# Kernel optimization log

Measured on AMD Instinct MI355X. Metric: run time of the kernel, lower is better.

The kernel has to match this reference:

```python
import jax, jax.numpy as jnp
import numpy as np

B, T, W_IN = 64, 512, 40
KS = 3
N = KS * KS          # 9 sampling points
CF = 8               # conv filters
GH = 32              # GRU hidden
GIN = (W_IN - KS + 1) * CF  # 304
ATTN = 32


def setup_inputs() -> dict:
    key = jax.random.key(0)
    ks = jax.random.split(key, 10)
    p = {}
    p["x"] = jax.random.normal(ks[0], (B, 1, T, W_IN), jnp.float32)
    p["p_w"] = jax.random.normal(ks[1], (2 * N, 1, KS, KS), jnp.float32) * 0.01
    p["p_b"] = jnp.zeros((2 * N,), jnp.float32)
    p["dcn_w"] = jax.random.normal(ks[2], (CF, 1, KS, KS), jnp.float32) * 0.1
    p["dcn_b"] = jnp.zeros((CF,), jnp.float32)
    p["w_ih"] = jax.random.normal(ks[3], (3 * GH, GIN), jnp.float32) * 0.05
    p["w_hh"] = jax.random.normal(ks[4], (3 * GH, GH), jnp.float32) * 0.05
    p["b_ih"] = jnp.zeros((3 * GH,), jnp.float32)
    p["b_hh"] = jnp.zeros((3 * GH,), jnp.float32)
    p["w1"] = jax.random.normal(ks[5], (ATTN, GH), jnp.float32) * 0.1
    p["b1"] = jnp.zeros((ATTN,), jnp.float32)
    p["w2"] = jax.random.normal(ks[6], (GH, ATTN), jnp.float32) * 0.1
    p["b2"] = jnp.zeros((GH,), jnp.float32)
    p["w3"] = jax.random.normal(ks[7], (2, GH), jnp.float32) * 0.1
    p["b3"] = jnp.zeros((2,), jnp.float32)
    return p


def _deform_conv(x, p_w, p_b, w, b):
    # x: (B,1,H,W). Deform-conv v1: offsets from a VALID 3x3 conv, bilinear gather.
    Bb, C, H, W = x.shape
    offset = jax.lax.conv_general_dilated(
        x, p_w, (1, 1), "VALID",
        dimension_numbers=("NCHW", "OIHW", "NCHW")) + p_b[None, :, None, None]
    h, w_ = offset.shape[2], offset.shape[3]  # (T-2, 38)
    r = KS // 2
    pny, pnx = jnp.meshgrid(jnp.arange(-r, r + 1), jnp.arange(-r, r + 1), indexing="ij")
    p0y, p0x = jnp.meshgrid(jnp.arange(1, h + 1), jnp.arange(1, w_ + 1), indexing="ij")
    py = offset[:, :N] + pny.reshape(1, N, 1, 1) + p0y[None, None]  # (B,N,h,w)
    px = offset[:, N:] + pnx.reshape(1, N, 1, 1) + p0x[None, None]
    py = jnp.clip(py, 0.0, H - 1.0)
    px = jnp.clip(px, 0.0, W - 1.0)
    y0 = jnp.floor(py).astype(jnp.int32)
    x0 = jnp.floor(px).astype(jnp.int32)
    y1 = jnp.minimum(y0 + 1, H - 1)
    x1 = jnp.minimum(x0 + 1, W - 1)
    wy = (py - y0)[:, None]  # (B,1,N,h,w)
    wx = (px - x0)[:, None]
    flat = x.reshape(Bb, C, H * W)

    def gather(yi, xi):
        idx = (yi * W + xi).reshape(Bb, 1, -1)
        g = jnp.take_along_axis(flat, idx, axis=2)
        return g.reshape(Bb, C, N, h, w_)

    g00 = gather(y0, x0); g01 = gather(y0, x1)
    g10 = gather(y1, x0); g11 = gather(y1, x1)
    samp = (g00 * (1 - wy) * (1 - wx) + g01 * (1 - wy) * wx
            + g10 * wy * (1 - wx) + g11 * wy * wx)  # (B,C,N,h,w)
    out = jnp.einsum("bcnhw,ocn->bohw", samp, w.reshape(w.shape[0], C, N))
    return out + b[None, :, None, None]


def _gru(seq, w_ih, w_hh, b_ih, b_hh):
    # seq: (T,B,GIN); PyTorch GRU equations, single layer, h0 = 0
    xp = jnp.einsum("tbi,hi->tbh", seq, w_ih) + b_ih  # (T,B,3H)
    h0 = jnp.zeros((seq.shape[1], GH), seq.dtype)

    def step(hprev, xt):
        hp = hprev @ w_hh.T + b_hh
        xr, xz, xn = jnp.split(xt, 3, axis=-1)
        hr, hz, hn = jnp.split(hp, 3, axis=-1)
        rg = jax.nn.sigmoid(xr + hr)
        zg = jax.nn.sigmoid(xz + hz)
        ng = jnp.tanh(xn + rg * hn)
        hnew = (1 - zg) * ng + zg * hprev
        return hnew, hnew

    _, ys = jax.lax.scan(step, h0, xp)
    return ys  # (T,B,GH)


def _forward(x, p_w, p_b, dcn_w, dcn_b, w_ih, w_hh, b_ih, b_hh, w1, b1, w2, b2, w3, b3):
    y = _deform_conv(x, p_w, p_b, dcn_w, dcn_b)        # (B,CF,h,w)
    h = y.shape[2]
    y = jnp.transpose(y, (2, 0, 3, 1)).reshape(h, y.shape[1], -1)  # wait
    return y


def _model(x, p_w, p_b, dcn_w, dcn_b, w_ih, w_hh, b_ih, b_hh, w1, b1, w2, b2, w3, b3):
    y = _deform_conv(x, p_w, p_b, dcn_w, dcn_b)        # (B,CF,h,w)
    Bb = y.shape[0]
    h = y.shape[2]
    seq = jnp.transpose(y, (2, 0, 3, 1)).reshape(h, Bb, -1)  # (h,B,w*CF) w-major then channel
    enc = jnp.transpose(_gru(seq, w_ih, w_hh, b_ih, b_hh), (1, 0, 2))  # (B,h,GH)
    a = jnp.tanh(enc @ w1.T + b1) @ w2.T + b2          # (B,h,GH)
    a = jax.nn.softmax(a, axis=1)                      # softmax over time
    pooled = jnp.sum(a * enc, axis=1)                  # (B,GH)
    return pooled @ w3.T + b3                          # (B,2)


def reference(x, p_w, p_b, dcn_w, dcn_b, w_ih, w_hh, b_ih, b_hh, w1, b1, w2, b2, w3, b3):
    return _model(x, p_w, p_b, dcn_w, dcn_b, w_ih, w_hh, b_ih, b_hh, w1, b1, w2, b2, w3, b3)
```

## Files before the change

kernel.cpp:

```cpp
#include <hip/hip_runtime.h>
#include <math.h>
#include <stdint.h>

#define BB 64
#define TT 512
#define W_IN 40
#define CF 8
#define GH 32
#define HOUT 510
#define WOUT 38
#define GIN 304
#define G3 96
#define ATT 32
#define MROWS (HOUT * BB)

#define LOG2E 1.4426950408889634f

__device__ __forceinline__ float fast_rcp(float x) {
#if defined(__has_builtin)
# if __has_builtin(__builtin_amdgcn_rcpf)
    return __builtin_amdgcn_rcpf(x);
# else
    return 1.f / x;
# endif
#else
    return 1.f / x;
#endif
}

__device__ __forceinline__ float fast_exp2(float x) {
#if defined(__has_builtin)
# if __has_builtin(__builtin_amdgcn_exp2f)
    return __builtin_amdgcn_exp2f(x);
# else
    return exp2f(x);
# endif
#else
    return exp2f(x);
#endif
}

typedef __attribute__((address_space(3))) uint32_t lds_u32_t;
typedef const __attribute__((address_space(1))) uint32_t glb_u32_t;

#if defined(__has_builtin) && __has_builtin(__builtin_amdgcn_global_load_lds)
#define HAS_GLL 1
#else
#define HAS_GLL 0
#endif

#define KC2 152
#define WI_C 19
__global__ __launch_bounds__(192, 1) void k_dcn_gemm_fused(
    const float* __restrict__ x, const float* __restrict__ p_w, const float* __restrict__ p_b,
    const float* __restrict__ dcn_w, const float* __restrict__ dcn_b,
    const float* __restrict__ w_ih, const float* __restrict__ b_ih,
    float* __restrict__ xp)
{
    __shared__ float As[128 * KC2];
    __shared__ float Ws[96 * KC2];
    __shared__ float pw_s[162], pb_s[18], dw_s[72], db_s[8];

    const int tid = threadIdx.x;
    const int t0  = blockIdx.x * 2;
    const int r0  = blockIdx.x * 128;
    const int mg  = tid / 12;
    const int ng  = tid % 12;

    if (tid < 162) pw_s[tid] = p_w[tid];
    if (tid < 18)  pb_s[tid] = p_b[tid];
    if (tid < 72)  dw_s[tid] = dcn_w[tid];
    if (tid < 8)   db_s[tid] = dcn_b[tid];

    float bih[8];
    #pragma unroll
    for (int j = 0; j < 8; ++j) bih[j] = b_ih[ng + 12 * j];

    float acc[8][8];
    #pragma unroll
    for (int i = 0; i < 8; ++i)
        #pragma unroll
        for (int j = 0; j < 8; ++j) acc[i][j] = 0.f;

    auto stageW = [&](int ch) {
        for (int u4 = tid; u4 < 96 * (KC2 / 4); u4 += 192) {
            const int g   = u4 / (KC2 / 4);
            const int k4l = u4 % (KC2 / 4);
            const float* src = w_ih + (size_t)g * GIN + ch * KC2 + k4l * 4;
            float* dst = &Ws[u4 * 4];
#if HAS_GLL
            __builtin_amdgcn_global_load_lds((glb_u32_t*)(uintptr_t)src,
                                             (lds_u32_t*)(uintptr_t)dst, 16, 0, 0);
#else
            *(float4*)dst = *(const float4*)src;
#endif
        }
    };

    auto phaseA = [&](int ch) {
        for (int item = tid; item < 128 * WI_C; item += 192) {
            const int lr = item / WI_C;
            const int wl = item % WI_C;
            const int wi = ch * WI_C + wl;
            const int t  = t0 + (lr >> 6);
            const int b  = lr & 63;
            const float* xb = x + (size_t)b * TT * W_IN;

            float patch[9];
            #pragma unroll
            for (int ky = 0; ky < 3; ++ky)
                #pragma unroll
                for (int kx = 0; kx < 3; ++kx)
                    patch[ky * 3 + kx] = xb[(t + ky) * W_IN + wi + kx];

            float offs[18];
            #pragma unroll
            for (int n = 0; n < 18; ++n) {
                float a = pb_s[n];
                #pragma unroll
                for (int k = 0; k < 9; ++k) a += patch[k] * pw_s[n * 9 + k];
                offs[n] = a;
            }

            float samp[9];
            #pragma unroll
            for (int n = 0; n < 9; ++n) {
                float py = offs[n]     + (float)(n / 3 - 1) + (float)(t + 1);
                float px = offs[9 + n] + (float)(n % 3 - 1) + (float)(wi + 1);
                py = fminf(fmaxf(py, 0.f), (float)(TT - 1));
                px = fminf(fmaxf(px, 0.f), (float)(W_IN - 1));
                float fy = floorf(py), fx = floorf(px);
                int y0 = (int)fy, x0 = (int)fx;
                int y1 = min(y0 + 1, TT - 1), x1 = min(x0 + 1, W_IN - 1);
                float wy = py - fy, wx = px - fx;
                float g00 = xb[y0 * W_IN + x0], g01 = xb[y0 * W_IN + x1];
                float g10 = xb[y1 * W_IN + x0], g11 = xb[y1 * W_IN + x1];
                samp[n] = g00 * (1.f - wy) * (1.f - wx) + g01 * (1.f - wy) * wx
                        + g10 * wy * (1.f - wx) + g11 * wy * wx;
            }

            float o[CF];
            #pragma unroll
            for (int c = 0; c < CF; ++c) {
                float a = db_s[c];
                #pragma unroll
                for (int n = 0; n < 9; ++n) a += samp[n] * dw_s[c * 9 + n];
                o[c] = a;
            }
            float* arow = &As[lr * KC2 + wl * 8];
            ((float4*)arow)[0] = make_float4(o[0], o[1], o[2], o[3]);
            ((float4*)arow)[1] = make_float4(o[4], o[5], o[6], o[7]);
        }
    };

    auto gemm = [&]() {
        #pragma unroll 2
        for (int k4 = 0; k4 < KC2 / 4; ++k4) {
            float4 a[8], w[8];
            #pragma unroll
            for (int i = 0; i < 8; ++i)
                a[i] = *(const float4*)&As[(mg + 16 * i) * KC2 + k4 * 4];
            #pragma unroll
            for (int j = 0; j < 8; ++j)
                w[j] = *(const float4*)&Ws[(ng + 12 * j) * KC2 + k4 * 4];
            #pragma unroll
            for (int i = 0; i < 8; ++i)
                #pragma unroll
                for (int j = 0; j < 8; ++j)
                    acc[i][j] += a[i].x * w[j].x + a[i].y * w[j].y
                               + a[i].z * w[j].z + a[i].w * w[j].w;
        }
    };

    __syncthreads();
    stageW(0);
    phaseA(0);
    __syncthreads();
    gemm();
    __syncthreads();
    stageW(1);
    phaseA(1);
    __syncthreads();
    gemm();

    #pragma unroll
    for (int i = 0; i < 8; ++i) {
        const int row = r0 + mg + 16 * i;
        #pragma unroll
        for (int j = 0; j < 8; ++j)
            xp[(size_t)row * G3 + ng + 12 * j] = acc[i][j] + bih[j];
    }
}

#define GCH 16
#define NCH 32

__global__ __launch_bounds__(64) void k_gru(
    const float* __restrict__ xp, const float* __restrict__ w_hh,
    const float* __restrict__ b_hh, float* __restrict__ enc)
{
    __shared__ float xs[2][GCH * G3];

    const int l = threadIdx.x;
    const int half = l >> 5;
    const int j = l & 31;
    const int b = blockIdx.x;

    float wr[16], wz[16], wn[16];
    #pragma unroll
    for (int i = 0; i < 16; ++i) {
        wr[i] = w_hh[(size_t)j * GH + half * 16 + i];
        wz[i] = w_hh[(size_t)(GH + j) * GH + half * 16 + i];
        wn[i] = w_hh[(size_t)(2 * GH + j) * GH + half * 16 + i];
    }
    const float br = b_hh[j], bz = b_hh[GH + j], bn = b_hh[2 * GH + j];

    auto stage = [&](int c, int buf) {
        #pragma unroll
        for (int k = 0; k < 6; ++k) {
            const int f  = k * 256 + l * 4;
            const int tl = f / 96;
            const int g  = f % 96;
            int gt = c * GCH + tl;
            if (gt > HOUT - 1) gt = HOUT - 1;
            const float* src = xp + ((size_t)gt * BB + b) * G3 + g;
            float* dst = &xs[buf][k * 256];
#if HAS_GLL
            __builtin_amdgcn_global_load_lds((glb_u32_t*)(uintptr_t)src,
                                             (lds_u32_t*)(uintptr_t)dst, 16, 0, 0);
#else
            *(float4*)(&xs[buf][f]) = *(const float4*)src;
#endif
        }
    };

    stage(0, 0);
    float h = 0.f;

    #pragma unroll 1
    for (int c = 0; c < NCH; ++c) {
        const int buf = c & 1;
        if (c + 1 < NCH) {
            stage(c + 1, buf ^ 1);
            asm volatile("s_waitcnt vmcnt(6)" ::: "memory");
        } else {
            asm volatile("s_waitcnt vmcnt(0)" ::: "memory");
        }
        const int nst = (c == NCH - 1) ? (HOUT - (NCH - 1) * GCH) : GCH;
        #pragma unroll 1
        for (int tl = 0; tl < nst; ++tl) {
            const float* xrow = &xs[buf][tl * G3];
            const float xr = xrow[j], xz = xrow[GH + j], xn = xrow[2 * GH + j];

            float pr0 = 0.f, pr1 = 0.f, pr2 = 0.f, pr3 = 0.f;
            float pz0 = 0.f, pz1 = 0.f, pz2 = 0.f, pz3 = 0.f;
            float pn0 = 0.f, pn1 = 0.f, pn2 = 0.f, pn3 = 0.f;
            #pragma unroll
            for (int i = 0; i < 16; i += 4) {
                const float h0 = __shfl(h, half * 16 + i + 0, 64);
                const float h1 = __shfl(h, half * 16 + i + 1, 64);
                const float h2 = __shfl(h, half * 16 + i + 2, 64);
                const float h3 = __shfl(h, half * 16 + i + 3, 64);
                pr0 += wr[i + 0] * h0; pr1 += wr[i + 1] * h1;
                pr2 += wr[i + 2] * h2; pr3 += wr[i + 3] * h3;
                pz0 += wz[i + 0] * h0; pz1 += wz[i + 1] * h1;
                pz2 += wz[i + 2] * h2; pz3 += wz[i + 3] * h3;
                pn0 += wn[i + 0] * h0; pn1 += wn[i + 1] * h1;
                pn2 += wn[i + 2] * h2; pn3 += wn[i + 3] * h3;
            }
            const float pr = (pr0 + pr1) + (pr2 + pr3);
            const float pz = (pz0 + pz1) + (pz2 + pz3);
            const float pn = (pn0 + pn1) + (pn2 + pn3);
            const float ar = br + pr + __shfl_xor(pr, 32, 64);
            const float az = bz + pz + __shfl_xor(pz, 32, 64);
            const float an = bn + pn + __shfl_xor(pn, 32, 64);

            const float rg = fast_rcp(1.f + fast_exp2(-(xr + ar) * LOG2E));
            const float zg = fast_rcp(1.f + fast_exp2(-(xz + az) * LOG2E));
            const float pre = xn + rg * an;
            const float e2 = fast_exp2(pre * (2.f * LOG2E));
            const float tg = 1.f - 2.f * fast_rcp(e2 + 1.f);
            h = (1.f - zg) * tg + zg * h;

            const int t = c * GCH + tl;
            if (!half) enc[((size_t)b * HOUT + t) * GH + j] = h;
        }
    }
}

__global__ __launch_bounds__(256) void k_attn_part(
    const float* __restrict__ enc,
    const float* __restrict__ w1, const float* __restrict__ b1,
    const float* __restrict__ w2, const float* __restrict__ b2,
    float* __restrict__ part)
{
    __shared__ float w1s[ATT * 33], w2s[GH * 33];
    __shared__ float b1s[ATT], b2s[GH];
    __shared__ float encs[8][GH], apres[8][ATT];
    __shared__ float rm[8 * GH], rs[8 * GH], rp[8 * GH];

    const int b   = blockIdx.x >> 2;
    const int c   = blockIdx.x & 3;
    const int tid = threadIdx.x;
    const int ttl = tid >> 5;
    const int j   = tid & 31;

    for (int i = tid; i < ATT * GH; i += 256) {
        int r = i >> 5, cc = i & 31;
        w1s[r * 33 + cc] = w1[i];
        w2s[r * 33 + cc] = w2[i];
    }
    if (tid < ATT)           b1s[tid] = b1[tid];
    else if (tid < ATT + GH) b2s[tid - ATT] = b2[tid - ATT];
    __syncthreads();

    const int tbeg = c * 128;
    const int tend = min(HOUT, tbeg + 128);

    float m = -INFINITY, s = 0.f, p = 0.f;
    const float* encb = enc + (size_t)b * HOUT * GH;

    for (int t0 = tbeg; t0 < tend; t0 += 8) {
        const int t = t0 + ttl;
        const bool act = (t < tend);
        const float ev = act ? encb[t * GH + j] : 0.f;
        encs[ttl][j] = ev;
        __syncthreads();

        float a1 = b1s[j];
        #pragma unroll
        for (int k = 0; k < GH; ++k) a1 += encs[ttl][k] * w1s[j * 33 + k];
        apres[ttl][j] = tanhf(a1);
        __syncthreads();

        float a2 = b2s[j];
        #pragma unroll
        for (int k = 0; k < ATT; ++k) a2 += apres[ttl][k] * w2s[j * 33 + k];

        if (act) {
            float mn = fmaxf(m, a2);
            float sc = expf(m - mn);
            float e  = expf(a2 - mn);
            s = s * sc + e;
            p = p * sc + e * ev;
            m = mn;
        }
        __syncthreads();
    }

    rm[tid] = m; rs[tid] = s; rp[tid] = p;
    __syncthreads();

    if (tid < GH) {
        float M = -INFINITY;
        #pragma unroll
        for (int q = 0; q < 8; ++q) M = fmaxf(M, rm[q * GH + tid]);
        float S = 0.f, P = 0.f;
        #pragma unroll
        for (int q = 0; q < 8; ++q) {
            float sc = expf(rm[q * GH + tid] - M);
            S += rs[q * GH + tid] * sc;
            P += rp[q * GH + tid] * sc;
        }
        float* pb = part + ((size_t)b * 4 + c) * 96;
        pb[tid] = M; pb[32 + tid] = S; pb[64 + tid] = P;
    }
}

__global__ __launch_bounds__(64) void k_attn_fin(
    const float* __restrict__ part,
    const float* __restrict__ w3, const float* __restrict__ b3,
    float* __restrict__ out)
{
    __shared__ float pooled[GH];
    const int b = blockIdx.x;
    const int tid = threadIdx.x;

    if (tid < GH) {
        const float* pb = part + (size_t)b * 4 * 96;
        float M = -INFINITY;
        #pragma unroll
        for (int c = 0; c < 4; ++c) M = fmaxf(M, pb[c * 96 + tid]);
        float S = 0.f, P = 0.f;
        #pragma unroll
        for (int c = 0; c < 4; ++c) {
            float sc = expf(pb[c * 96 + tid] - M);
            S += pb[c * 96 + 32 + tid] * sc;
            P += pb[c * 96 + 64 + tid] * sc;
        }
        pooled[tid] = P / S;
    }
    __syncthreads();

    if (tid < 2) {
        float a = b3[tid];
        #pragma unroll
        for (int k = 0; k < GH; ++k) a += pooled[k] * w3[tid * GH + k];
        out[b * 2 + tid] = a;
    }
}

extern "C" void kernel_launch(void* const* d_in, const int* in_sizes, int n_in,
                              void* d_out, int out_size, void* d_ws, size_t ws_size,
                              hipStream_t stream)
{
    const float* x     = (const float*)d_in[0];
    const float* p_w   = (const float*)d_in[1];
    const float* p_b   = (const float*)d_in[2];
    const float* dcn_w = (const float*)d_in[3];
    const float* dcn_b = (const float*)d_in[4];
    const float* w_ih  = (const float*)d_in[5];
    const float* w_hh  = (const float*)d_in[6];
    const float* b_ih  = (const float*)d_in[7];
    const float* b_hh  = (const float*)d_in[8];
    const float* w1    = (const float*)d_in[9];
    const float* b1    = (const float*)d_in[10];
    const float* w2    = (const float*)d_in[11];
    const float* b2    = (const float*)d_in[12];
    const float* w3    = (const float*)d_in[13];
    const float* b3    = (const float*)d_in[14];
    float* out = (float*)d_out;

    const size_t XP_F = (size_t)MROWS * G3;
    float* xp   = (float*)d_ws;
    float* enc  = xp + XP_F;
    float* part = xp;

    hipLaunchKernelGGL(k_dcn_gemm_fused, dim3(MROWS / 128), dim3(192), 0, stream,
                       x, p_w, p_b, dcn_w, dcn_b, w_ih, b_ih, xp);
    hipLaunchKernelGGL(k_gru, dim3(BB), dim3(64), 0, stream,
                       xp, w_hh, b_hh, enc);
    hipLaunchKernelGGL(k_attn_part, dim3(BB * 4), dim3(256), 0, stream,
                       enc, w1, b1, w2, b2, part);
    hipLaunchKernelGGL(k_attn_fin, dim3(BB), dim3(64), 0, stream,
                       part, w3, b3, out);
}
```

Measured before the change: 380.4 us.

## Split DCN and input GEMM, use LDS hidden state in GRU, tile attention

The fused deform-conv+GEMM kernel is split into a standalone DCN kernel that caches input rows in LDS and writes the seq buffer, followed by a separate 128-row GEMM kernel, when workspace is large enough. The GRU now broadcasts the hidden state through shared memory with float4 reads instead of per-element shuffles. The attention partial kernel processes 64-step tiles with double-buffered encoder loads, so it needs fewer barriers. The split adds a round trip of the large seq intermediate through global memory. The GRU writes hs without a barrier and relies on the block being a single wave.

```diff
diff --git a/kernel.cpp b/kernel.cpp
--- a/kernel.cpp
+++ b/kernel.cpp
@@ -48,6 +48,168 @@
 #else
 #define HAS_GLL 0
 #endif
+
+__global__ __launch_bounds__(256) void k_dcn_lds(
+    const float* __restrict__ x, const float* __restrict__ p_w, const float* __restrict__ p_b,
+    const float* __restrict__ dcn_w, const float* __restrict__ dcn_b,
+    float* __restrict__ seq)
+{
+    __shared__ float xt[36 * W_IN];
+    __shared__ float pw_s[162], pb_s[18], dw_s[72], db_s[8];
+
+    const int tid  = threadIdx.x;
+    const int b    = blockIdx.x >> 4;
+    const int q    = blockIdx.x & 15;
+    const int base = 32 * q - 1;
+
+    if (tid < 162) pw_s[tid] = p_w[tid];
+    if (tid < 18)  pb_s[tid] = p_b[tid];
+    if (tid < 72)  dw_s[tid] = dcn_w[tid];
+    if (tid < 8)   db_s[tid] = dcn_b[tid];
+
+    const float* xb = x + (size_t)b * TT * W_IN;
+    for (int u = tid; u < 360; u += 256) {
+        const int r  = u / 10;
+        const int c4 = (u % 10) * 4;
+        const int grow = min(max(base + r, 0), TT - 1);
+        *(float4*)&xt[r * W_IN + c4] = *(const float4*)&xb[grow * W_IN + c4];
+    }
+    __syncthreads();
+
+    for (int it = tid; it < 32 * WOUT; it += 256) {
+        const int tl = it / WOUT;
+        const int wi = it % WOUT;
+        const int t  = 32 * q + tl;
+        const int lt = tl + 1;
+
+        float patch[9];
+        #pragma unroll
+        for (int ky = 0; ky < 3; ++ky)
+            #pragma unroll
+            for (int kx = 0; kx < 3; ++kx)
+                patch[ky * 3 + kx] = xt[(lt + ky) * W_IN + wi + kx];
+
+        float offs[18];
+        #pragma unroll
+        for (int n = 0; n < 18; ++n) {
+            float a = pb_s[n];
+            #pragma unroll
+            for (int k = 0; k < 9; ++k) a += patch[k] * pw_s[n * 9 + k];
+            offs[n] = a;
+        }
+
+        float samp[9];
+        #pragma unroll
+        for (int n = 0; n < 9; ++n) {
+            float py = offs[n]     + (float)(n / 3 - 1) + (float)(t + 1);
+            float px = offs[9 + n] + (float)(n % 3 - 1) + (float)(wi + 1);
+            py = fminf(fmaxf(py, 0.f), (float)(TT - 1));
+            px = fminf(fmaxf(px, 0.f), (float)(W_IN - 1));
+            float fy = floorf(py), fx = floorf(px);
+            int y0 = (int)fy, x0 = (int)fx;
+            int y1 = min(y0 + 1, TT - 1), x1 = min(x0 + 1, W_IN - 1);
+            float wy = py - fy, wx = px - fx;
+            int ly0 = min(max(y0 - base, 0), 35);
+            int ly1 = min(max(y1 - base, 0), 35);
+            float g00 = xt[ly0 * W_IN + x0], g01 = xt[ly0 * W_IN + x1];
+            float g10 = xt[ly1 * W_IN + x0], g11 = xt[ly1 * W_IN + x1];
+            samp[n] = g00 * (1.f - wy) * (1.f - wx) + g01 * (1.f - wy) * wx
+                    + g10 * wy * (1.f - wx) + g11 * wy * wx;
+        }
+
+        float o[CF];
+        #pragma unroll
+        for (int c = 0; c < CF; ++c) {
+            float a = db_s[c];
+            #pragma unroll
+            for (int n = 0; n < 9; ++n) a += samp[n] * dw_s[c * 9 + n];
+            o[c] = a;
+        }
+        float* srow = seq + ((size_t)t * BB + b) * GIN + wi * CF;
+        ((float4*)srow)[0] = make_float4(o[0], o[1], o[2], o[3]);
+        ((float4*)srow)[1] = make_float4(o[4], o[5], o[6], o[7]);
+    }
+}
+
+#define KC 76
+__global__ __launch_bounds__(128) void k_gemm(
+    const float* __restrict__ seq, const float* __restrict__ w_ih,
+    const float* __restrict__ b_ih, float* __restrict__ xp)
+{
+    __shared__ float As[128 * KC];
+    __shared__ float Ws[96 * 84];
+
+    const int tid = threadIdx.x;
+    const int mg = tid >> 3;
+    const int ng = tid & 7;
+    const int r0 = blockIdx.x * 128;
+
+    float bih[12];
+    #pragma unroll
+    for (int j = 0; j < 12; ++j) bih[j] = b_ih[ng + 8 * j];
+
+    float acc[8][12];
+    #pragma unroll
+    for (int i = 0; i < 8; ++i)
+        #pragma unroll
+        for (int j = 0; j < 12; ++j) acc[i][j] = 0.f;
+
+    #pragma unroll 1
+    for (int ch = 0; ch < 4; ++ch) {
+        const int kc = ch * KC;
+        #pragma unroll 1
+        for (int p = 0; p < 19; ++p) {
+            const int u4 = tid + p * 128;
+            const int m  = u4 / (KC / 4);
+            const int k4 = u4 % (KC / 4);
+            const float* src = seq + ((size_t)(r0 + m)) * GIN + kc + k4 * 4;
+            float* dst = &As[u4 * 4];
+#if HAS_GLL
+            __builtin_amdgcn_global_load_lds((glb_u32_t*)(uintptr_t)src,
+                                             (lds_u32_t*)(uintptr_t)dst, 16, 0, 0);
+#else
+            *(float4*)dst = *(const float4*)src;
+#endif
+        }
+        #pragma unroll 1
+        for (int p = 0; p < 15; ++p) {
+            const int u4 = tid + p * 128;
+            if (u4 < 96 * (KC / 4)) {
+                const int row = u4 / (KC / 4);
+                const int k4  = u4 % (KC / 4);
+                float4 v = *(const float4*)(w_ih + (size_t)row * GIN + kc + k4 * 4);
+                *(float4*)&Ws[row * 84 + k4 * 4] = v;
+            }
+        }
+        __syncthreads();
+
+        #pragma unroll 2
+        for (int k4 = 0; k4 < KC / 4; ++k4) {
+            float4 a[8], w[12];
+            #pragma unroll
+            for (int i = 0; i < 8; ++i)
+                a[i] = *(const float4*)&As[(mg + 16 * i) * KC + k4 * 4];
+            #pragma unroll
+            for (int j = 0; j < 12; ++j)
+                w[j] = *(const float4*)&Ws[(ng + 8 * j) * 84 + k4 * 4];
+            #pragma unroll
+            for (int i = 0; i < 8; ++i)
+                #pragma unroll
+                for (int j = 0; j < 12; ++j)
+                    acc[i][j] += a[i].x * w[j].x + a[i].y * w[j].y
+                               + a[i].z * w[j].z + a[i].w * w[j].w;
+        }
+        __syncthreads();
+    }
+
+    #pragma unroll
+    for (int i = 0; i < 8; ++i) {
+        const int row = r0 + mg + 16 * i;
+        #pragma unroll
+        for (int j = 0; j < 12; ++j)
+            xp[(size_t)row * G3 + ng + 8 * j] = acc[i][j] + bih[j];
+    }
+}
 
 #define KC2 152
 #define WI_C 19
@@ -200,6 +362,7 @@
     const float* __restrict__ b_hh, float* __restrict__ enc)
 {
     __shared__ float xs[2][GCH * G3];
+    __shared__ float hs[GH];
 
     const int l = threadIdx.x;
     const int half = l >> 5;
@@ -214,6 +377,8 @@
         wn[i] = w_hh[(size_t)(2 * GH + j) * GH + half * 16 + i];
     }
     const float br = b_hh[j], bz = b_hh[GH + j], bn = b_hh[2 * GH + j];
+
+    hs[j] = 0.f;
 
     auto stage = [&](int c, int buf) {
         #pragma unroll
@@ -252,25 +417,28 @@
             const float* xrow = &xs[buf][tl * G3];
             const float xr = xrow[j], xz = xrow[GH + j], xn = xrow[2 * GH + j];
 
-            float pr0 = 0.f, pr1 = 0.f, pr2 = 0.f, pr3 = 0.f;
-            float pz0 = 0.f, pz1 = 0.f, pz2 = 0.f, pz3 = 0.f;
-            float pn0 = 0.f, pn1 = 0.f, pn2 = 0.f, pn3 = 0.f;
+            float4 h0 = *(const float4*)&hs[half * 16];
+            float4 h1 = *(const float4*)&hs[half * 16 + 4];
+            float4 h2 = *(const float4*)&hs[half * 16 + 8];
+            float4 h3 = *(const float4*)&hs[half * 16 + 12];
+            float hv[16] = {h0.x,h0.y,h0.z,h0.w, h1.x,h1.y,h1.z,h1.w,
+                            h2.x,h2.y,h2.z,h2.w, h3.x,h3.y,h3.z,h3.w};
+
+            float pr0=0.f,pr1=0.f,pr2=0.f,pr3=0.f;
+            float pz0=0.f,pz1=0.f,pz2=0.f,pz3=0.f;
+            float pn0=0.f,pn1=0.f,pn2=0.f,pn3=0.f;
             #pragma unroll
             for (int i = 0; i < 16; i += 4) {
-                const float h0 = __shfl(h, half * 16 + i + 0, 64);
-                const float h1 = __shfl(h, half * 16 + i + 1, 64);
-                const float h2 = __shfl(h, half * 16 + i + 2, 64);
-                const float h3 = __shfl(h, half * 16 + i + 3, 64);
-                pr0 += wr[i + 0] * h0; pr1 += wr[i + 1] * h1;
-                pr2 += wr[i + 2] * h2; pr3 += wr[i + 3] * h3;
-                pz0 += wz[i + 0] * h0; pz1 += wz[i + 1] * h1;
-                pz2 += wz[i + 2] * h2; pz3 += wz[i + 3] * h3;
-                pn0 += wn[i + 0] * h0; pn1 += wn[i + 1] * h1;
-                pn2 += wn[i + 2] * h2; pn3 += wn[i + 3] * h3;
+                pr0 += wr[i+0]*hv[i+0]; pr1 += wr[i+1]*hv[i+1];
+                pr2 += wr[i+2]*hv[i+2]; pr3 += wr[i+3]*hv[i+3];
+                pz0 += wz[i+0]*hv[i+0]; pz1 += wz[i+1]*hv[i+1];
+                pz2 += wz[i+2]*hv[i+2]; pz3 += wz[i+3]*hv[i+3];
+                pn0 += wn[i+0]*hv[i+0]; pn1 += wn[i+1]*hv[i+1];
+                pn2 += wn[i+2]*hv[i+2]; pn3 += wn[i+3]*hv[i+3];
             }
-            const float pr = (pr0 + pr1) + (pr2 + pr3);
-            const float pz = (pz0 + pz1) + (pz2 + pz3);
-            const float pn = (pn0 + pn1) + (pn2 + pn3);
+            const float pr = (pr0+pr1)+(pr2+pr3);
+            const float pz = (pz0+pz1)+(pz2+pz3);
+            const float pn = (pn0+pn1)+(pn2+pn3);
             const float ar = br + pr + __shfl_xor(pr, 32, 64);
             const float az = bz + pz + __shfl_xor(pz, 32, 64);
             const float an = bn + pn + __shfl_xor(pn, 32, 64);
@@ -281,6 +449,8 @@
             const float e2 = fast_exp2(pre * (2.f * LOG2E));
             const float tg = 1.f - 2.f * fast_rcp(e2 + 1.f);
             h = (1.f - zg) * tg + zg * h;
+
+            hs[j] = h;
 
             const int t = c * GCH + tl;
             if (!half) enc[((size_t)b * HOUT + t) * GH + j] = h;
@@ -296,13 +466,14 @@
 {
     __shared__ float w1s[ATT * 33], w2s[GH * 33];
     __shared__ float b1s[ATT], b2s[GH];
-    __shared__ float encs[8][GH], apres[8][ATT];
-    __shared__ float rm[8 * GH], rs[8 * GH], rp[8 * GH];
+    __shared__ float e2[2][64 * 36];
+    __shared__ float ap[64 * 33];
+    __shared__ float rm[256], rs[256], rp[256];
 
     const int b   = blockIdx.x >> 2;
     const int c   = blockIdx.x & 3;
     const int tid = threadIdx.x;
-    const int ttl = tid >> 5;
+    const int tl  = tid >> 5;
     const int j   = tid & 31;
 
     for (int i = tid; i < ATT * GH; i += 256) {
@@ -312,38 +483,66 @@
     }
     if (tid < ATT)           b1s[tid] = b1[tid];
     else if (tid < ATT + GH) b2s[tid - ATT] = b2[tid - ATT];
-    __syncthreads();
-
-    const int tbeg = c * 128;
-    const int tend = min(HOUT, tbeg + 128);
 
     float m = -INFINITY, s = 0.f, p = 0.f;
     const float* encb = enc + (size_t)b * HOUT * GH;
 
-    for (int t0 = tbeg; t0 < tend; t0 += 8) {
-        const int t = t0 + ttl;
-        const bool act = (t < tend);
-        const float ev = act ? encb[t * GH + j] : 0.f;
-        encs[ttl][j] = ev;
+    {
+        const int tbase = c * 128;
+        for (int u = tid; u < 512; u += 256) {
+            const int r = u >> 3, c4 = (u & 7) * 4;
+            const int t = tbase + r;
+            float4 v = make_float4(0.f, 0.f, 0.f, 0.f);
+            if (t < HOUT) v = *(const float4*)&encb[t * GH + c4];
+            *(float4*)&e2[0][r * 36 + c4] = v;
+        }
+    }
+    __syncthreads();
+
+    #pragma unroll 1
+    for (int tile = 0; tile < 2; ++tile) {
+        const int buf = tile & 1;
+        const int tbase = c * 128 + tile * 64;
+
+        #pragma unroll
+        for (int sIt = 0; sIt < 8; ++sIt) {
+            const int tloc = sIt * 8 + tl;
+            float a1 = b1s[j];
+            #pragma unroll
+            for (int k = 0; k < GH; ++k)
+                a1 += e2[buf][tloc * 36 + k] * w1s[j * 33 + k];
+            ap[tloc * 33 + j] = tanhf(a1);
+        }
         __syncthreads();
 
-        float a1 = b1s[j];
-        #pragma unroll
-        for (int k = 0; k < GH; ++k) a1 += encs[ttl][k] * w1s[j * 33 + k];
-        apres[ttl][j] = tanhf(a1);
-        __syncthreads();
-
-        float a2 = b2s[j];
-        #pragma unroll
-        for (int k = 0; k < ATT; ++k) a2 += apres[ttl][k] * w2s[j * 33 + k];
-
-        if (act) {
-            float mn = fmaxf(m, a2);
-            float sc = expf(m - mn);
-            float e  = expf(a2 - mn);
-            s = s * sc + e;
-            p = p * sc + e * ev;
-            m = mn;
+        if (tile == 0) {
+            const int nb = c * 128 + 64;
+            for (int u = tid; u < 512; u += 256) {
+                const int r = u >> 3, c4 = (u & 7) * 4;
+                const int t = nb + r;
+                float4 v = make_float4(0.f, 0.f, 0.f, 0.f);
+                if (t < HOUT) v = *(const float4*)&encb[t * GH + c4];
+                *(float4*)&e2[1][r * 36 + c4] = v;
+            }
+        }
+
+        #pragma unroll
+        for (int sIt = 0; sIt < 8; ++sIt) {
+            const int tloc = sIt * 8 + tl;
+            const int t = tbase + tloc;
+            float a2 = b2s[j];
+            #pragma unroll
+            for (int k = 0; k < ATT; ++k)
+                a2 += ap[tloc * 33 + k] * w2s[j * 33 + k];
+            if (t < HOUT) {
+                const float ev = e2[buf][tloc * 36 + j];
+                float mn = fmaxf(m, a2);
+                float sc = expf(m - mn);
+                float e  = expf(a2 - mn);
+                s = s * sc + e;
+                p = p * sc + e * ev;
+                m = mn;
+            }
         }
         __syncthreads();
     }
@@ -354,13 +553,13 @@
     if (tid < GH) {
         float M = -INFINITY;
         #pragma unroll
-        for (int q = 0; q < 8; ++q) M = fmaxf(M, rm[q * GH + tid]);
+        for (int qq = 0; qq < 8; ++qq) M = fmaxf(M, rm[qq * GH + tid]);
         float S = 0.f, P = 0.f;
         #pragma unroll
-        for (int q = 0; q < 8; ++q) {
-            float sc = expf(rm[q * GH + tid] - M);
-            S += rs[q * GH + tid] * sc;
-            P += rp[q * GH + tid] * sc;
+        for (int qq = 0; qq < 8; ++qq) {
+            float sc = expf(rm[qq * GH + tid] - M);
+            S += rs[qq * GH + tid] * sc;
+            P += rp[qq * GH + tid] * sc;
         }
         float* pb = part + ((size_t)b * 4 + c) * 96;
         pb[tid] = M; pb[32 + tid] = S; pb[64 + tid] = P;
@@ -421,17 +620,36 @@
     const float* b3    = (const float*)d_in[14];
     float* out = (float*)d_out;
 
-    const size_t XP_F = (size_t)MROWS * G3;
-    float* xp   = (float*)d_ws;
-    float* enc  = xp + XP_F;
-    float* part = xp;
-
-    hipLaunchKernelGGL(k_dcn_gemm_fused, dim3(MROWS / 128), dim3(192), 0, stream,
-                       x, p_w, p_b, dcn_w, dcn_b, w_ih, b_ih, xp);
-    hipLaunchKernelGGL(k_gru, dim3(BB), dim3(64), 0, stream,
-                       xp, w_hh, b_hh, enc);
-    hipLaunchKernelGGL(k_attn_part, dim3(BB * 4), dim3(256), 0, stream,
-                       enc, w1, b1, w2, b2, part);
-    hipLaunchKernelGGL(k_attn_fin, dim3(BB), dim3(64), 0, stream,
-                       part, w3, b3, out);
-}
+    const size_t SEQ_F = (size_t)MROWS * GIN;
+    const size_t XP_F  = (size_t)MROWS * G3;
+    const size_t ENC_F = (size_t)BB * HOUT * GH;
+
+    if (ws_size >= (SEQ_F + XP_F) * sizeof(float)) {
+        float* seq  = (float*)d_ws;
+        float* xp   = seq + SEQ_F;
+        float* enc  = seq;
+        float* part = seq + ENC_F;
+        hipLaunchKernelGGL(k_dcn_lds, dim3(BB * 16), dim3(256), 0, stream,
+                           x, p_w, p_b, dcn_w, dcn_b, seq);
+        hipLaunchKernelGGL(k_gemm, dim3(MROWS / 128), dim3(128), 0, stream,
+                           seq, w_ih, b_ih, xp);
+        hipLaunchKernelGGL(k_gru, dim3(BB), dim3(64), 0, stream,
+                           xp, w_hh, b_hh, enc);
+        hipLaunchKernelGGL(k_attn_part, dim3(BB * 4), dim3(256), 0, stream,
+                           enc, w1, b1, w2, b2, part);
+        hipLaunchKernelGGL(k_attn_fin, dim3(BB), dim3(64), 0, stream,
+                           part, w3, b3, out);
+    } else {
+        float* xp   = (float*)d_ws;
+        float* enc  = xp + XP_F;
+        float* part = xp;
+        hipLaunchKernelGGL(k_dcn_gemm_fused, dim3(MROWS / 128), dim3(192), 0, stream,
+                           x, p_w, p_b, dcn_w, dcn_b, w_ih, b_ih, xp);
+        hipLaunchKernelGGL(k_gru, dim3(BB), dim3(64), 0, stream,
+                           xp, w_hh, b_hh, enc);
+        hipLaunchKernelGGL(k_attn_part, dim3(BB * 4), dim3(256), 0, stream,
+                           enc, w1, b1, w2, b2, part);
+        hipLaunchKernelGGL(k_attn_fin, dim3(BB), dim3(64), 0, stream,
+                           part, w3, b3, out);
+    }
+}
```

After: 405.9 us. +6.7%, slower.
